# Kernel optimization log

Hardware: AMD Instinct MI355X
Metric: run time of the kernel (lower is better)

Reference implementation:

```python
import jax, jax.numpy as jnp
import numpy as np

B, N, D, H, C, K = 4096, 64, 128, 256, 8, 3
L = N * D  # latent_dim = num_patches * d_model = 8192
UQ, LQ = 0.9, 0.1


def setup_inputs() -> dict:
    key = jax.random.key(0)
    ks = jax.random.split(key, 6)
    z = jax.random.normal(ks[0], (B, N, D), dtype=jnp.float32)
    q = jax.random.uniform(ks[1], (B,), dtype=jnp.float32)
    ch_ids = jax.random.randint(ks[2], (B,), 0, C, dtype=jnp.int32)
    # Xavier-style init for the 3 expert MLPs (Linear(L,H), Linear(H,L)) + heads Linear(L,1)
    s1 = float(np.sqrt(2.0 / (L + H)))
    s2 = float(np.sqrt(2.0 / (H + L)))
    sh = float(np.sqrt(2.0 / (L + 1)))
    W1 = jax.random.normal(ks[3], (K, L, H), dtype=jnp.float32) * s1
    W2 = jax.random.normal(ks[4], (K, H, L), dtype=jnp.float32) * s2
    Wh = jax.random.normal(ks[5], (K, L), dtype=jnp.float32) * sh
    return dict(z=z, q=q, ch_ids=ch_ids,
                W1=W1, b1=jnp.zeros((K, H), jnp.float32),
                W2=W2, b2=jnp.zeros((K, L), jnp.float32),
                Wh=Wh, bh=jnp.zeros((K,), jnp.float32))


def _channel_thresholds(q, ch_ids):
    """Per-channel sample-adjusted upper/lower quantiles, torch.quantile(..., interpolation='lower')."""
    def one(c):
        mask = ch_ids == c
        n = jnp.sum(mask).astype(jnp.float32)
        s = jnp.sort(jnp.where(mask, q, jnp.inf))  # channel values occupy first n slots
        au = jnp.ceil((n + 1.0) * UQ) / n
        pu = jnp.where(au > 1.0, UQ, au)
        al = jnp.floor((n + 1.0) * LQ) / n
        pl = jnp.where(al < 0.0, LQ, al)
        iu = jnp.floor(pu * (n - 1.0)).astype(jnp.int32)  # 'lower' interpolation index
        il = jnp.floor(pl * (n - 1.0)).astype(jnp.int32)
        return s[iu], s[il]
    return jax.vmap(one)(jnp.arange(C))  # (C,), (C,)


def reference(z, q, ch_ids, W1, b1, W2, b2, Wh, bh):
    uq_th, lq_th = _channel_thresholds(q, ch_ids)
    group = jnp.where(q <= lq_th[ch_ids], 2,
                      jnp.where(q >= uq_th[ch_ids], 0, 1)).astype(jnp.int32)  # (B,)
    zf = z.reshape(z.shape[0], -1)  # (B, L) -- Flatten(start_dim=-2)

    def expert(w1, c1, w2, c2, wh, ch):
        h = jax.nn.gelu(zf @ w1 + c1, approximate=False)   # (B, H)
        o = h @ w2 + c2                                     # (B, L)
        return o @ wh + ch                                  # (B,)

    logits_all = jax.vmap(expert)(W1, b1, W2, b2, Wh, bh)   # (K, B)
    logits = jnp.take_along_axis(logits_all, group[None, :], axis=0)[0]  # (B,)

    # per-channel softmax over logits (stable), matching torch.softmax on each channel's indices
    m = jax.ops.segment_max(logits, ch_ids, num_segments=C)
    e = jnp.exp(logits - m[ch_ids])
    ssum = jax.ops.segment_sum(e, ch_ids, num_segments=C)
    qwa_coeff = e / ssum[ch_ids]
    refined_probs = q * qwa_coeff
    return refined_probs
```

## Files before the change

kernel.cpp:

```cpp
#include <hip/hip_runtime.h>

typedef unsigned short u16;
typedef unsigned int u32;
typedef __attribute__((ext_vector_type(8))) short short8;
typedef __attribute__((ext_vector_type(4))) float f32x4;

#define NB 4096
#define LDIM 8192
#define HDIM 256
#define NEXP 3
#define NCH 8

__device__ inline u16 f2bf(float f) {
  u32 u = __float_as_uint(f);
  u += 0x7FFFu + ((u >> 16) & 1u);
  return (u16)(u >> 16);
}
__device__ inline u32 pack2(float x, float y) {
  return (u32)f2bf(x) | ((u32)f2bf(y) << 16);
}

__global__ void thresh_kernel(const float* __restrict__ q, const int* __restrict__ ch,
                              float* __restrict__ uq_th, float* __restrict__ lq_th) {
  int c = blockIdx.x;
  int tid = threadIdx.x;
  __shared__ float vals[1536];
  __shared__ int oidx[1536];
  __shared__ int n_sh;
  if (tid == 0) n_sh = 0;
  __syncthreads();
  for (int i = tid; i < NB; i += 256) {
    if (ch[i] == c) {
      int p = atomicAdd(&n_sh, 1);
      if (p < 1536) { vals[p] = q[i]; oidx[p] = i; }
    }
  }
  __syncthreads();
  int n = n_sh < 1536 ? n_sh : 1536;
  float nf = (float)n_sh;
  float au = ceilf((nf + 1.0f) * 0.9f) / nf;
  float pu = (au > 1.0f) ? 0.9f : au;
  int iu = (int)floorf(pu * (nf - 1.0f));
  float al = floorf((nf + 1.0f) * 0.1f) / nf;
  float pl = (al < 0.0f) ? 0.1f : al;
  int il = (int)floorf(pl * (nf - 1.0f));
  for (int e = tid; e < n; e += 256) {
    float v = vals[e];
    int oi = oidx[e];
    int r = 0;
    for (int m = 0; m < n; ++m) {
      float vm = vals[m];
      if (vm < v || (vm == v && oidx[m] < oi)) r++;
    }
    if (r == iu) uq_th[c] = v;
    if (r == il) lq_th[c] = v;
  }
}

__global__ void group_kernel(const float* __restrict__ q, const int* __restrict__ ch,
                             const float* __restrict__ uq_th, const float* __restrict__ lq_th,
                             int* __restrict__ group, int* __restrict__ cnt, int* __restrict__ idxl) {
  int b = blockIdx.x * 256 + threadIdx.x;
  if (b >= NB) return;
  float qq = q[b];
  int c = ch[b];
  int g = (qq <= lq_th[c]) ? 2 : ((qq >= uq_th[c]) ? 0 : 1);
  group[b] = g;
  int pos = atomicAdd(&cnt[g], 1);
  idxl[g * NB + pos] = b;
}

__global__ void v_kernel(const float* __restrict__ W2, const float* __restrict__ Wh,
                         float* __restrict__ v) {
  int wv = blockIdx.x * 4 + (threadIdx.x >> 6);
  int lane = threadIdx.x & 63;
  int k = wv >> 8, h = wv & 255;
  const float4* w2 = (const float4*)(W2 + ((size_t)k * HDIM + h) * LDIM);
  const float4* wh = (const float4*)(Wh + (size_t)k * LDIM);
  float s = 0.f;
  for (int i = lane; i < LDIM / 4; i += 64) {
    float4 a = w2[i], b = wh[i];
    s += a.x * b.x + a.y * b.y + a.z * b.z + a.w * b.w;
  }
  for (int off = 32; off; off >>= 1) s += __shfl_down(s, off);
  if (lane == 0) v[k * HDIM + h] = s;
}

__global__ void cbias_kernel(const float* __restrict__ b2, const float* __restrict__ Wh,
                             const float* __restrict__ bh, float* __restrict__ cbias) {
  int k = threadIdx.x >> 6, lane = threadIdx.x & 63;
  float s = 0.f;
  for (int l = lane; l < LDIM; l += 64) s += b2[k * LDIM + l] * Wh[k * LDIM + l];
  for (int off = 32; off; off >>= 1) s += __shfl_down(s, off);
  if (lane == 0) cbias[k] = s + bh[k];
}

__global__ void transpose_kernel(const float* __restrict__ W1, u16* __restrict__ W1t) {
  __shared__ float tile[32][33];
  int k = blockIdx.z;
  int l0 = blockIdx.x * 32;
  int h0 = blockIdx.y * 32;
  int t = threadIdx.x;
  const float* src = W1 + (size_t)k * LDIM * HDIM;
  u16* dst = W1t + (size_t)k * HDIM * LDIM;
#pragma unroll
  for (int r = 0; r < 4; ++r) {
    int ll = r * 8 + (t >> 5);
    int hh = t & 31;
    tile[ll][hh] = src[(size_t)(l0 + ll) * HDIM + h0 + hh];
  }
  __syncthreads();
#pragma unroll
  for (int r = 0; r < 4; ++r) {
    int hh = r * 8 + (t >> 5);
    int ll = t & 31;
    dst[(size_t)(h0 + hh) * LDIM + l0 + ll] = f2bf(tile[ll][hh]);
  }
}

__global__ void __launch_bounds__(256) gemm_kernel(
    const float* __restrict__ z, const u16* __restrict__ W1t,
    const float* __restrict__ b1, const int* __restrict__ idxl,
    const int* __restrict__ cnt, const float* __restrict__ v,
    float* __restrict__ logits) {
  int kexp = blockIdx.z;
  int nk = cnt[kexp];
  int rowbase = blockIdx.x * 64;
  if (rowbase >= nk) return;
  int h0 = blockIdx.y * 64;
  int tid = threadIdx.x;

  __shared__ __align__(16) u16 As[64 * 64];
  __shared__ __align__(16) u16 Bs[64 * 64];
  __shared__ float Ps[64 * 65];

  const int* idxk = idxl + kexp * NB;
  int r0 = tid >> 3;
  int r1 = r0 + 32;
  int kg = tid & 7;
  int p0 = rowbase + r0; if (p0 > nk - 1) p0 = nk - 1;
  int p1 = rowbase + r1; if (p1 > nk - 1) p1 = nk - 1;
  const float* zr0 = z + (size_t)idxk[p0] * LDIM + kg * 8;
  const float* zr1 = z + (size_t)idxk[p1] * LDIM + kg * 8;
  const u16* w0 = W1t + ((size_t)kexp * HDIM + h0 + r0) * LDIM + kg * 8;
  const u16* w1 = W1t + ((size_t)kexp * HDIM + h0 + r1) * LDIM + kg * 8;
  int sw0 = r0 * 64 + ((kg * 8) ^ ((r0 & 7) * 8));
  int sw1 = r1 * 64 + ((kg * 8) ^ ((r1 & 7) * 8));

  int lane = tid & 63;
  int wv = tid >> 6;
  int wr = (wv >> 1) * 32;
  int wc = (wv & 1) * 32;
  int fr = lane & 15;
  int kgl = (lane >> 4) * 8;

  f32x4 acc[2][2] = {};

  for (int kt = 0; kt < LDIM; kt += 64) {
    float4 a0 = *(const float4*)(zr0 + kt);
    float4 a1 = *(const float4*)(zr0 + kt + 4);
    float4 a2 = *(const float4*)(zr1 + kt);
    float4 a3 = *(const float4*)(zr1 + kt + 4);
    uint4 bw0 = *(const uint4*)(w0 + kt);
    uint4 bw1 = *(const uint4*)(w1 + kt);
    uint4 pa0, pa1;
    pa0.x = pack2(a0.x, a0.y); pa0.y = pack2(a0.z, a0.w);
    pa0.z = pack2(a1.x, a1.y); pa0.w = pack2(a1.z, a1.w);
    pa1.x = pack2(a2.x, a2.y); pa1.y = pack2(a2.z, a2.w);
    pa1.z = pack2(a3.x, a3.y); pa1.w = pack2(a3.z, a3.w);
    *(uint4*)&As[sw0] = pa0;
    *(uint4*)&As[sw1] = pa1;
    *(uint4*)&Bs[sw0] = bw0;
    *(uint4*)&Bs[sw1] = bw1;
    __syncthreads();
#pragma unroll
    for (int ks = 0; ks < 2; ++ks) {
      int kk = ks * 32 + kgl;
      int ra0 = wr + fr, ra1 = wr + 16 + fr;
      int ca0 = wc + fr, ca1 = wc + 16 + fr;
      short8 af0 = *(const short8*)&As[ra0 * 64 + (kk ^ ((ra0 & 7) * 8))];
      short8 af1 = *(const short8*)&As[ra1 * 64 + (kk ^ ((ra1 & 7) * 8))];
      short8 bf0 = *(const short8*)&Bs[ca0 * 64 + (kk ^ ((ca0 & 7) * 8))];
      short8 bf1 = *(const short8*)&Bs[ca1 * 64 + (kk ^ ((ca1 & 7) * 8))];
      acc[0][0] = __builtin_amdgcn_mfma_f32_16x16x32_bf16(af0, bf0, acc[0][0], 0, 0, 0);
      acc[0][1] = __builtin_amdgcn_mfma_f32_16x16x32_bf16(af0, bf1, acc[0][1], 0, 0, 0);
      acc[1][0] = __builtin_amdgcn_mfma_f32_16x16x32_bf16(af1, bf0, acc[1][0], 0, 0, 0);
      acc[1][1] = __builtin_amdgcn_mfma_f32_16x16x32_bf16(af1, bf1, acc[1][1], 0, 0, 0);
    }
    __syncthreads();
  }

  const float* b1g = b1 + kexp * HDIM + h0;
  const float* vg = v + kexp * HDIM + h0;
  float bc[2], vc[2];
#pragma unroll
  for (int cb = 0; cb < 2; ++cb) {
    int col = wc + cb * 16 + fr;
    bc[cb] = b1g[col];
    vc[cb] = vg[col];
  }
#pragma unroll
  for (int rb = 0; rb < 2; ++rb)
#pragma unroll
    for (int cb = 0; cb < 2; ++cb)
#pragma unroll
      for (int i = 0; i < 4; ++i) {
        int row = wr + rb * 16 + (lane >> 4) * 4 + i;
        int col = wc + cb * 16 + fr;
        float x = acc[rb][cb][i] + bc[cb];
        float g = 0.5f * x * (1.0f + erff(x * 0.70710678118654752f));
        Ps[row * 65 + col] = g * vc[cb];
      }
  __syncthreads();
  if (tid < 64) {
    int p = rowbase + tid;
    if (p < nk) {
      float s = 0.f;
#pragma unroll 8
      for (int j = 0; j < 64; ++j) s += Ps[tid * 65 + j];
      atomicAdd(&logits[idxk[p]], s);
    }
  }
}

__global__ void softmax_kernel(const float* __restrict__ logits, const float* __restrict__ cbias,
                               const int* __restrict__ group, const float* __restrict__ q,
                               const int* __restrict__ ch, float* __restrict__ out) {
  int c = blockIdx.x;
  int tid = threadIdx.x;
  __shared__ float red[256];
  float m = -3.4e38f;
  for (int i = tid; i < NB; i += 256)
    if (ch[i] == c) {
      float x = logits[i] + cbias[group[i]];
      m = fmaxf(m, x);
    }
  red[tid] = m;
  __syncthreads();
  for (int s = 128; s > 0; s >>= 1) {
    if (tid < s) red[tid] = fmaxf(red[tid], red[tid + s]);
    __syncthreads();
  }
  m = red[0];
  __syncthreads();
  float sum = 0.f;
  for (int i = tid; i < NB; i += 256)
    if (ch[i] == c) sum += expf(logits[i] + cbias[group[i]] - m);
  red[tid] = sum;
  __syncthreads();
  for (int s = 128; s > 0; s >>= 1) {
    if (tid < s) red[tid] += red[tid + s];
    __syncthreads();
  }
  float S = red[0];
  for (int i = tid; i < NB; i += 256)
    if (ch[i] == c) out[i] = q[i] * expf(logits[i] + cbias[group[i]] - m) / S;
}

extern "C" void kernel_launch(void* const* d_in, const int* in_sizes, int n_in,
                              void* d_out, int out_size, void* d_ws, size_t ws_size,
                              hipStream_t stream) {
  const float* z  = (const float*)d_in[0];
  const float* q  = (const float*)d_in[1];
  const int*   ch = (const int*)d_in[2];
  const float* W1 = (const float*)d_in[3];
  const float* b1 = (const float*)d_in[4];
  const float* W2 = (const float*)d_in[5];
  const float* b2 = (const float*)d_in[6];
  const float* Wh = (const float*)d_in[7];
  const float* bh = (const float*)d_in[8];
  float* out = (float*)d_out;

  float* wsf    = (float*)d_ws;
  float* logits = wsf;
  int*   cnt    = (int*)(wsf + 4096);
  float* uq_th  = wsf + 4100;
  float* lq_th  = wsf + 4108;
  float* cbias  = wsf + 4116;
  float* v      = wsf + 4120;
  int*   group  = (int*)(wsf + 4888);
  int*   idxl   = (int*)(wsf + 8984);
  u16*   W1t    = (u16*)(wsf + 21272);

  hipMemsetAsync(d_ws, 0, 16400, stream);
  hipLaunchKernelGGL(thresh_kernel, dim3(NCH), dim3(256), 0, stream, q, ch, uq_th, lq_th);
  hipLaunchKernelGGL(group_kernel, dim3(16), dim3(256), 0, stream, q, ch, uq_th, lq_th, group, cnt, idxl);
  hipLaunchKernelGGL(v_kernel, dim3(192), dim3(256), 0, stream, W2, Wh, v);
  hipLaunchKernelGGL(cbias_kernel, dim3(1), dim3(192), 0, stream, b2, Wh, bh, cbias);
  hipLaunchKernelGGL(transpose_kernel, dim3(256, 8, 3), dim3(256), 0, stream, W1, W1t);
  hipLaunchKernelGGL(gemm_kernel, dim3(64, 4, 3), dim3(256), 0, stream, z, W1t, b1, idxl, cnt, v, logits);
  hipLaunchKernelGGL(softmax_kernel, dim3(NCH), dim3(256), 0, stream, logits, cbias, group, q, ch, out);
}
```

Before: 610.9 us.

## Split-K the grouped GEMM with double-buffered LDS loads and a separate epilogue kernel

The GEMM is split along the reduction dimension into four slices. This raises the grid from 768 blocks to 3072 so that more CUs are busy. Partial sums go to a workspace buffer, and a new per-row epilogue kernel adds the slices, applies bias and GELU, and reduces against v. The logits atomics and the large memset go away. The main loop now double-buffers LDS, using global_load_lds for W1t and prefetching the z tile in registers, and the W1 transpose uses 64x64 tiles with vectorized bf16 stores. In exchange it adds about 16MB of partial-sum write and read traffic plus an extra launch.

```diff
diff --git a/kernel.cpp b/kernel.cpp
--- a/kernel.cpp
+++ b/kernel.cpp
@@ -10,6 +10,10 @@
 #define HDIM 256
 #define NEXP 3
 #define NCH 8
+#define KSPLIT 4
+#define KSLICE (LDIM / KSPLIT)
+#define BK 64
+#define NT (KSLICE / BK)
 
 __device__ inline u16 f2bf(float f) {
   u32 u = __float_as_uint(f);
@@ -18,6 +22,10 @@
 }
 __device__ inline u32 pack2(float x, float y) {
   return (u32)f2bf(x) | ((u32)f2bf(y) << 16);
+}
+__device__ inline void gll16(const void* g, void* l) {
+  __builtin_amdgcn_global_load_lds((const __attribute__((address_space(1))) void*)g,
+                                   (__attribute__((address_space(3))) void*)l, 16, 0, 0);
 }
 
 __global__ void thresh_kernel(const float* __restrict__ q, const int* __restrict__ ch,
@@ -96,109 +104,135 @@
 }
 
 __global__ void transpose_kernel(const float* __restrict__ W1, u16* __restrict__ W1t) {
-  __shared__ float tile[32][33];
+  __shared__ float tile[64][65];
   int k = blockIdx.z;
-  int l0 = blockIdx.x * 32;
-  int h0 = blockIdx.y * 32;
+  int l0 = blockIdx.x * 64;
+  int h0 = blockIdx.y * 64;
   int t = threadIdx.x;
-  const float* src = W1 + (size_t)k * LDIM * HDIM;
-  u16* dst = W1t + (size_t)k * HDIM * LDIM;
-#pragma unroll
-  for (int r = 0; r < 4; ++r) {
-    int ll = r * 8 + (t >> 5);
-    int hh = t & 31;
-    tile[ll][hh] = src[(size_t)(l0 + ll) * HDIM + h0 + hh];
-  }
-  __syncthreads();
-#pragma unroll
-  for (int r = 0; r < 4; ++r) {
-    int hh = r * 8 + (t >> 5);
-    int ll = t & 31;
-    dst[(size_t)(h0 + hh) * LDIM + l0 + ll] = f2bf(tile[ll][hh]);
+  const float* src = W1 + (size_t)k * LDIM * HDIM + (size_t)l0 * HDIM + h0;
+  u16* dst = W1t + (size_t)k * HDIM * LDIM + (size_t)h0 * LDIM + l0;
+  int hr = t & 63, lr = t >> 6;
+#pragma unroll
+  for (int p = 0; p < 16; ++p) {
+    int l = p * 4 + lr;
+    tile[l][hr] = src[(size_t)l * HDIM + hr];
+  }
+  __syncthreads();
+  int cw = t & 7, hw = t >> 3;
+#pragma unroll
+  for (int p = 0; p < 2; ++p) {
+    int h = p * 32 + hw;
+    short8 v8;
+#pragma unroll
+    for (int j = 0; j < 8; ++j) v8[j] = (short)f2bf(tile[cw * 8 + j][h]);
+    *(short8*)&dst[(size_t)h * LDIM + cw * 8] = v8;
   }
 }
 
 __global__ void __launch_bounds__(256) gemm_kernel(
     const float* __restrict__ z, const u16* __restrict__ W1t,
-    const float* __restrict__ b1, const int* __restrict__ idxl,
-    const int* __restrict__ cnt, const float* __restrict__ v,
-    float* __restrict__ logits) {
-  int kexp = blockIdx.z;
+    const int* __restrict__ idxl, const int* __restrict__ cnt,
+    float* __restrict__ part) {
+  int zid = blockIdx.z;
+  int kexp = zid >> 2, s = zid & 3;
   int nk = cnt[kexp];
   int rowbase = blockIdx.x * 64;
   if (rowbase >= nk) return;
   int h0 = blockIdx.y * 64;
   int tid = threadIdx.x;
-
-  __shared__ __align__(16) u16 As[64 * 64];
-  __shared__ __align__(16) u16 Bs[64 * 64];
-  __shared__ float Ps[64 * 65];
+  int lane = tid & 63, wv = tid >> 6;
+
+  __shared__ __align__(16) u16 As[2][4096];
+  __shared__ __align__(16) u16 Bs[2][4096];
+  __shared__ int sidx[64];
 
   const int* idxk = idxl + kexp * NB;
-  int r0 = tid >> 3;
-  int r1 = r0 + 32;
-  int kg = tid & 7;
+  if (tid < 64) {
+    int p = rowbase + tid;
+    sidx[tid] = idxk[p < nk ? p : nk - 1];
+  }
+
+  int r0 = tid >> 3, r1 = r0 + 32, kg = tid & 7;
   int p0 = rowbase + r0; if (p0 > nk - 1) p0 = nk - 1;
   int p1 = rowbase + r1; if (p1 > nk - 1) p1 = nk - 1;
-  const float* zr0 = z + (size_t)idxk[p0] * LDIM + kg * 8;
-  const float* zr1 = z + (size_t)idxk[p1] * LDIM + kg * 8;
-  const u16* w0 = W1t + ((size_t)kexp * HDIM + h0 + r0) * LDIM + kg * 8;
-  const u16* w1 = W1t + ((size_t)kexp * HDIM + h0 + r1) * LDIM + kg * 8;
-  int sw0 = r0 * 64 + ((kg * 8) ^ ((r0 & 7) * 8));
-  int sw1 = r1 * 64 + ((kg * 8) ^ ((r1 & 7) * 8));
-
-  int lane = tid & 63;
-  int wv = tid >> 6;
-  int wr = (wv >> 1) * 32;
-  int wc = (wv & 1) * 32;
-  int fr = lane & 15;
-  int kgl = (lane >> 4) * 8;
+  size_t kbase = (size_t)s * KSLICE;
+  const float* zr0 = z + (size_t)idxk[p0] * LDIM + kbase + kg * 8;
+  const float* zr1 = z + (size_t)idxk[p1] * LDIM + kbase + kg * 8;
+  int swA0 = r0 * 64 + ((kg * 8) ^ ((r0 & 7) * 8));
+  int swA1 = r1 * 64 + ((kg * 8) ^ ((r1 & 7) * 8));
+
+  const u16* bsrc0 = W1t + ((size_t)kexp * HDIM + h0 + wv * 16 + (lane >> 3)) * LDIM +
+                     kbase + (size_t)(((lane & 7) ^ (lane >> 3)) * 8);
+  const u16* bsrc1 = bsrc0 + 8 * LDIM;
+
+  int fr = lane & 15, kgl = (lane >> 4) * 8;
+  int wr = (wv >> 1) * 32, wc = (wv & 1) * 32;
+  int ra0 = wr + fr, ra1 = ra0 + 16, ca0 = wc + fr, ca1 = ca0 + 16;
+  int xA0 = (ra0 & 7) * 8, xA1 = (ra1 & 7) * 8, xB0 = (ca0 & 7) * 8, xB1 = (ca1 & 7) * 8;
 
   f32x4 acc[2][2] = {};
-
-  for (int kt = 0; kt < LDIM; kt += 64) {
-    float4 a0 = *(const float4*)(zr0 + kt);
-    float4 a1 = *(const float4*)(zr0 + kt + 4);
-    float4 a2 = *(const float4*)(zr1 + kt);
-    float4 a3 = *(const float4*)(zr1 + kt + 4);
-    uint4 bw0 = *(const uint4*)(w0 + kt);
-    uint4 bw1 = *(const uint4*)(w1 + kt);
+  float4 a0, a1, a2, a3;
+
+  {
+    char* lb = (char*)&Bs[0][0] + wv * 2048;
+    gll16(bsrc0, lb);
+    gll16(bsrc1, lb + 1024);
+    a0 = *(const float4*)(zr0);
+    a1 = *(const float4*)(zr0 + 4);
+    a2 = *(const float4*)(zr1);
+    a3 = *(const float4*)(zr1 + 4);
     uint4 pa0, pa1;
     pa0.x = pack2(a0.x, a0.y); pa0.y = pack2(a0.z, a0.w);
     pa0.z = pack2(a1.x, a1.y); pa0.w = pack2(a1.z, a1.w);
     pa1.x = pack2(a2.x, a2.y); pa1.y = pack2(a2.z, a2.w);
     pa1.z = pack2(a3.x, a3.y); pa1.w = pack2(a3.z, a3.w);
-    *(uint4*)&As[sw0] = pa0;
-    *(uint4*)&As[sw1] = pa1;
-    *(uint4*)&Bs[sw0] = bw0;
-    *(uint4*)&Bs[sw1] = bw1;
-    __syncthreads();
+    *(uint4*)&As[0][swA0] = pa0;
+    *(uint4*)&As[0][swA1] = pa1;
+  }
+  __syncthreads();
+
+  int cur = 0;
+  for (int t = 0; t < NT; ++t) {
+    int nxt = cur ^ 1;
+    bool pre = (t + 1 < NT);
+    if (pre) {
+      int off = (t + 1) * BK;
+      char* lb = (char*)&Bs[nxt][0] + wv * 2048;
+      gll16(bsrc0 + off, lb);
+      gll16(bsrc1 + off, lb + 1024);
+      a0 = *(const float4*)(zr0 + off);
+      a1 = *(const float4*)(zr0 + off + 4);
+      a2 = *(const float4*)(zr1 + off);
+      a3 = *(const float4*)(zr1 + off + 4);
+    }
+    const u16* Ac = &As[cur][0];
+    const u16* Bc = &Bs[cur][0];
 #pragma unroll
     for (int ks = 0; ks < 2; ++ks) {
       int kk = ks * 32 + kgl;
-      int ra0 = wr + fr, ra1 = wr + 16 + fr;
-      int ca0 = wc + fr, ca1 = wc + 16 + fr;
-      short8 af0 = *(const short8*)&As[ra0 * 64 + (kk ^ ((ra0 & 7) * 8))];
-      short8 af1 = *(const short8*)&As[ra1 * 64 + (kk ^ ((ra1 & 7) * 8))];
-      short8 bf0 = *(const short8*)&Bs[ca0 * 64 + (kk ^ ((ca0 & 7) * 8))];
-      short8 bf1 = *(const short8*)&Bs[ca1 * 64 + (kk ^ ((ca1 & 7) * 8))];
+      short8 af0 = *(const short8*)&Ac[ra0 * 64 + (kk ^ xA0)];
+      short8 af1 = *(const short8*)&Ac[ra1 * 64 + (kk ^ xA1)];
+      short8 bf0 = *(const short8*)&Bc[ca0 * 64 + (kk ^ xB0)];
+      short8 bf1 = *(const short8*)&Bc[ca1 * 64 + (kk ^ xB1)];
       acc[0][0] = __builtin_amdgcn_mfma_f32_16x16x32_bf16(af0, bf0, acc[0][0], 0, 0, 0);
       acc[0][1] = __builtin_amdgcn_mfma_f32_16x16x32_bf16(af0, bf1, acc[0][1], 0, 0, 0);
       acc[1][0] = __builtin_amdgcn_mfma_f32_16x16x32_bf16(af1, bf0, acc[1][0], 0, 0, 0);
       acc[1][1] = __builtin_amdgcn_mfma_f32_16x16x32_bf16(af1, bf1, acc[1][1], 0, 0, 0);
     }
+    if (pre) {
+      uint4 pa0, pa1;
+      pa0.x = pack2(a0.x, a0.y); pa0.y = pack2(a0.z, a0.w);
+      pa0.z = pack2(a1.x, a1.y); pa0.w = pack2(a1.z, a1.w);
+      pa1.x = pack2(a2.x, a2.y); pa1.y = pack2(a2.z, a2.w);
+      pa1.z = pack2(a3.x, a3.y); pa1.w = pack2(a3.z, a3.w);
+      *(uint4*)&As[nxt][swA0] = pa0;
+      *(uint4*)&As[nxt][swA1] = pa1;
+    }
     __syncthreads();
-  }
-
-  const float* b1g = b1 + kexp * HDIM + h0;
-  const float* vg = v + kexp * HDIM + h0;
-  float bc[2], vc[2];
-#pragma unroll
-  for (int cb = 0; cb < 2; ++cb) {
-    int col = wc + cb * 16 + fr;
-    bc[cb] = b1g[col];
-    vc[cb] = vg[col];
-  }
+    cur = nxt;
+  }
+
+  float* pdst = part + (size_t)s * NB * HDIM;
 #pragma unroll
   for (int rb = 0; rb < 2; ++rb)
 #pragma unroll
@@ -207,20 +241,29 @@
       for (int i = 0; i < 4; ++i) {
         int row = wr + rb * 16 + (lane >> 4) * 4 + i;
         int col = wc + cb * 16 + fr;
-        float x = acc[rb][cb][i] + bc[cb];
-        float g = 0.5f * x * (1.0f + erff(x * 0.70710678118654752f));
-        Ps[row * 65 + col] = g * vc[cb];
+        if (rowbase + row < nk)
+          pdst[(size_t)sidx[row] * HDIM + h0 + col] = acc[rb][cb][i];
       }
-  __syncthreads();
-  if (tid < 64) {
-    int p = rowbase + tid;
-    if (p < nk) {
-      float s = 0.f;
-#pragma unroll 8
-      for (int j = 0; j < 64; ++j) s += Ps[tid * 65 + j];
-      atomicAdd(&logits[idxk[p]], s);
-    }
-  }
+}
+
+__global__ void ep_kernel(const float* __restrict__ part, const float* __restrict__ b1,
+                          const float* __restrict__ v, const int* __restrict__ group,
+                          float* __restrict__ logits) {
+  int b = blockIdx.x;
+  int t = threadIdx.x;
+  int g = group[b];
+  size_t o = (size_t)b * HDIM + t;
+  const size_t SS = (size_t)NB * HDIM;
+  float x = part[o] + part[o + SS] + part[o + 2 * SS] + part[o + 3 * SS] + b1[g * HDIM + t];
+  float ge = 0.5f * x * (1.0f + erff(x * 0.70710678118654752f));
+  float y = ge * v[g * HDIM + t];
+#pragma unroll
+  for (int off = 32; off; off >>= 1) y += __shfl_down(y, off);
+  __shared__ float red[4];
+  int lane = t & 63, wv = t >> 6;
+  if (lane == 0) red[wv] = y;
+  __syncthreads();
+  if (t == 0) logits[b] = red[0] + red[1] + red[2] + red[3];
 }
 
 __global__ void softmax_kernel(const float* __restrict__ logits, const float* __restrict__ cbias,
@@ -281,13 +324,16 @@
   int*   group  = (int*)(wsf + 4888);
   int*   idxl   = (int*)(wsf + 8984);
   u16*   W1t    = (u16*)(wsf + 21272);
-
-  hipMemsetAsync(d_ws, 0, 16400, stream);
+  float* part   = wsf + 3167000;
+
+  hipMemsetAsync((char*)d_ws + 4096 * 4, 0, 16, stream);
   hipLaunchKernelGGL(thresh_kernel, dim3(NCH), dim3(256), 0, stream, q, ch, uq_th, lq_th);
   hipLaunchKernelGGL(group_kernel, dim3(16), dim3(256), 0, stream, q, ch, uq_th, lq_th, group, cnt, idxl);
   hipLaunchKernelGGL(v_kernel, dim3(192), dim3(256), 0, stream, W2, Wh, v);
   hipLaunchKernelGGL(cbias_kernel, dim3(1), dim3(192), 0, stream, b2, Wh, bh, cbias);
-  hipLaunchKernelGGL(transpose_kernel, dim3(256, 8, 3), dim3(256), 0, stream, W1, W1t);
-  hipLaunchKernelGGL(gemm_kernel, dim3(64, 4, 3), dim3(256), 0, stream, z, W1t, b1, idxl, cnt, v, logits);
+  hipLaunchKernelGGL(transpose_kernel, dim3(128, 4, 3), dim3(256), 0, stream, W1, W1t);
+  hipLaunchKernelGGL(gemm_kernel, dim3(64, 4, NEXP * KSPLIT), dim3(256), 0, stream,
+                     z, W1t, idxl, cnt, part);
+  hipLaunchKernelGGL(ep_kernel, dim3(NB), dim3(256), 0, stream, part, b1, v, group, logits);
   hipLaunchKernelGGL(softmax_kernel, dim3(NCH), dim3(256), 0, stream, logits, cbias, group, q, ch, out);
 }
```

After: 542.2 us. 11.2% less time.
